# Kernel optimization log

Measured on AMD Instinct MI355X. Metric: run time of the kernel, lower is better.

Reference implementation:

```python
import jax, jax.numpy as jnp
import numpy as np

PROCESSING_SPEED = 8.0  # init kwarg: softmax temperature
EPS = 1e-8              # torch F.cosine_similarity eps
BATCH, SIZE, DIM = 1024, 65536, 512


def setup_inputs() -> dict:
    key = jax.random.key(0)
    k1, k2 = jax.random.split(key)
    x = jax.random.normal(k1, (BATCH, DIM), dtype=jnp.float32)
    memory_bank = jax.random.normal(k2, (SIZE, DIM), dtype=jnp.float32)
    return {"x": x, "memory_bank": memory_bank}


def reference(x, memory_bank):
    # Cosine similarity between every query and every memory row, computed as
    # normalized dot products (math-equivalent to F.cosine_similarity with
    # denominator clamp max(||a||*||b||, eps), avoiding the (B,S,D) broadcast).
    x_norm = jnp.linalg.norm(x, axis=1, keepdims=True)            # (B, 1)
    m_norm = jnp.linalg.norm(memory_bank, axis=1, keepdims=True)  # (S, 1)
    dots = jnp.einsum('bd,sd->bs', x, memory_bank)                # (B, S)
    sims = dots / jnp.maximum(x_norm * m_norm.T, EPS)             # (B, S)
    attention = jax.nn.softmax(sims * PROCESSING_SPEED, axis=1)   # (B, S)
    return attention @ memory_bank                                # (B, D)
```

## Files before the change

### kernel.cpp

```cpp
#include <hip/hip_runtime.h>
#include <hip/hip_bf16.h>
#include <stdint.h>

#define B_N 1024
#define S_N 65536
#define D_N 512
#define NS 32
#define SC (S_N / NS)
#define SB 128
#define NSUB (SC / SB)

typedef __attribute__((ext_vector_type(8))) short bf16x8;
typedef __attribute__((ext_vector_type(4))) float f32x4;

#define OFF_MBF   ((size_t)0)
#define OFF_MT    (OFF_MBF + (size_t)S_N * D_N * 2)
#define OFF_XBF   (OFF_MT  + (size_t)D_N * S_N * 2)
#define OFF_RX    (OFF_XBF + (size_t)B_N * D_N * 2)
#define OFF_RM    (OFF_RX  + (size_t)B_N * 4)
#define OFF_LSUM  (OFF_RM  + (size_t)S_N * 4)
#define OFF_OPART (OFF_LSUM + (size_t)B_N * 4)

__device__ __forceinline__ unsigned short f2bf(float f) {
  unsigned u = __builtin_bit_cast(unsigned, f);
  u += 0x7fffu + ((u >> 16) & 1u);
  return (unsigned short)(u >> 16);
}

__device__ __forceinline__ void stage16(const unsigned short* g, unsigned short* l) {
  __builtin_amdgcn_global_load_lds(
      (const __attribute__((address_space(1))) void*)g,
      (__attribute__((address_space(3))) void*)l, 16, 0, 0);
}

__global__ void k_prep_x(const float* __restrict__ X, unsigned short* __restrict__ Xbf,
                         float* __restrict__ rx) {
  const int row = blockIdx.x;
  const int t = threadIdx.x;
  float4 v = ((const float4*)(X + (size_t)row * D_N))[t];
  float ss = v.x*v.x + v.y*v.y + v.z*v.z + v.w*v.w;
  ushort4 o; o.x = f2bf(v.x); o.y = f2bf(v.y); o.z = f2bf(v.z); o.w = f2bf(v.w);
  ((ushort4*)(Xbf + (size_t)row * D_N))[t] = o;
  #pragma unroll
  for (int m = 1; m < 64; m <<= 1) ss += __shfl_xor(ss, m);
  __shared__ float partial[2];
  if ((t & 63) == 0) partial[t >> 6] = ss;
  __syncthreads();
  if (t == 0) rx[row] = 11.541560327111707f * rsqrtf(fmaxf(partial[0] + partial[1], 1e-24f));
}

__global__ void k_prep_m(const float* __restrict__ M, unsigned short* __restrict__ Mbf,
                         unsigned short* __restrict__ Mt, float* __restrict__ rm) {
  __shared__ float ts[64 * 65];
  const int t = threadIdx.x;
  const int s0 = blockIdx.x * 64;
  const int r = t >> 2, cq = t & 3;
  const int c = t >> 2, sq = t & 3;
  float ss = 0.f;
  for (int ct = 0; ct < 8; ++ct) {
    float f[16];
    const float4* src = (const float4*)(M + (size_t)(s0 + r) * D_N + ct * 64 + cq * 16);
    #pragma unroll
    for (int k = 0; k < 4; ++k) {
      float4 v = src[k];
      f[4*k+0] = v.x; f[4*k+1] = v.y; f[4*k+2] = v.z; f[4*k+3] = v.w;
    }
    union { unsigned short u[16]; uint4 v4[2]; } pk;
    #pragma unroll
    for (int j = 0; j < 16; ++j) {
      ss += f[j] * f[j];
      pk.u[j] = f2bf(f[j]);
      ts[r * 65 + cq * 16 + j] = f[j];
    }
    uint4* dst = (uint4*)(Mbf + (size_t)(s0 + r) * D_N + ct * 64 + cq * 16);
    dst[0] = pk.v4[0]; dst[1] = pk.v4[1];
    __syncthreads();
    union { unsigned short u[16]; uint4 v4[2]; } pt;
    #pragma unroll
    for (int j = 0; j < 16; ++j) pt.u[j] = f2bf(ts[(sq * 16 + j) * 65 + c]);
    uint4* dt = (uint4*)(Mt + (size_t)(ct * 64 + c) * S_N + s0 + sq * 16);
    dt[0] = pt.v4[0]; dt[1] = pt.v4[1];
    __syncthreads();
  }
  ss += __shfl_xor(ss, 1);
  ss += __shfl_xor(ss, 2);
  if (cq == 0) rm[s0 + r] = rsqrtf(fmaxf(ss, 1e-24f));
}

__global__ __launch_bounds__(512, 2) void k_fused(
    const unsigned short* __restrict__ Xbf, const unsigned short* __restrict__ Mbf,
    const unsigned short* __restrict__ Mt, const float* __restrict__ rx,
    const float* __restrict__ rminv, float* __restrict__ lsum,
    float* __restrict__ Opart) {
  __shared__ unsigned short smem[16384];
  __shared__ unsigned short Ps[16384];

  const int t = threadIdx.x;
  const int w = t >> 6, lane = t & 63, quad = lane >> 4, l15 = lane & 15;
  const int qr = w >> 1, qc = w & 1;
  const int x7 = l15 & 7;

  const int bid = blockIdx.x;
  const int xcd = bid & 7, slot = bid >> 3;
  const int bblk = slot & 7;
  const int chunk = xcd * 4 + (slot >> 3);
  const int b0 = bblk * 128;
  const int s0 = chunk * SC;

  unsigned short* As = smem;
  unsigned short* Bs = smem + 8192;

  f32x4 accO[4][2][4];
  #pragma unroll
  for (int dc = 0; dc < 4; ++dc)
    #pragma unroll
    for (int i = 0; i < 2; ++i)
      #pragma unroll
      for (int j = 0; j < 4; ++j) accO[dc][i][j] = (f32x4){0.f, 0.f, 0.f, 0.f};

  float ls[4] = {0.f, 0.f, 0.f, 0.f};
  float rxj[4];
  #pragma unroll
  for (int j = 0; j < 4; ++j) rxj[j] = rx[b0 + qc * 64 + j * 16 + l15];

  const int srow8 = t >> 3;
  const int sch8  = ((t & 7) ^ (srow8 & 7)) * 8;
  const unsigned short* gX = Xbf + (size_t)(b0 + srow8) * D_N + sch8;
  const int mrow = t >> 4;
  const int mch  = ((t & 15) ^ (mrow & 7)) * 8;

  for (int sub = 0; sub < NSUB; ++sub) {
    const int sS = s0 + sub * SB;

    f32x4 accP[2][4];
    #pragma unroll
    for (int i = 0; i < 2; ++i)
      #pragma unroll
      for (int j = 0; j < 4; ++j) accP[i][j] = (f32x4){0.f, 0.f, 0.f, 0.f};

    const unsigned short* gM = Mbf + (size_t)(sS + srow8) * D_N + sch8;
    for (int k0 = 0; k0 < D_N; k0 += 64) {
      stage16(gM + k0,                      As + w * 512);
      stage16(gM + (size_t)64 * D_N + k0,   As + 4096 + w * 512);
      stage16(gX + k0,                      Bs + w * 512);
      stage16(gX + (size_t)64 * D_N + k0,   Bs + 4096 + w * 512);
      __syncthreads();
      #pragma unroll
      for (int kk = 0; kk < 64; kk += 32) {
        const int cq = (kk >> 3) + quad;
        bf16x8 a[2], b[4];
        #pragma unroll
        for (int i = 0; i < 2; ++i)
          a[i] = *(const bf16x8*)&As[(qr * 32 + i * 16 + l15) * 64 + ((cq ^ x7) << 3)];
        #pragma unroll
        for (int j = 0; j < 4; ++j)
          b[j] = *(const bf16x8*)&Bs[(qc * 64 + j * 16 + l15) * 64 + ((cq ^ x7) << 3)];
        #pragma unroll
        for (int i = 0; i < 2; ++i)
          #pragma unroll
          for (int j = 0; j < 4; ++j)
            accP[i][j] = __builtin_amdgcn_mfma_f32_16x16x32_bf16(a[i], b[j], accP[i][j], 0, 0, 0);
      }
      __syncthreads();
    }

    const float4 rm0 = *(const float4*)&rminv[sS + qr * 32 + quad * 4];
    const float4 rm1 = *(const float4*)&rminv[sS + qr * 32 + 16 + quad * 4];
    #pragma unroll
    for (int i = 0; i < 2; ++i) {
      const float4 rm = i ? rm1 : rm0;
      const int sl  = qr * 32 + i * 16 + quad * 4;
      const int c16 = sl >> 3;
      const int o8  = (sl >> 2) & 1;
      #pragma unroll
      for (int j = 0; j < 4; ++j) {
        const float p0 = exp2f(accP[i][j][0] * rxj[j] * rm.x);
        const float p1 = exp2f(accP[i][j][1] * rxj[j] * rm.y);
        const float p2 = exp2f(accP[i][j][2] * rxj[j] * rm.z);
        const float p3 = exp2f(accP[i][j][3] * rxj[j] * rm.w);
        ls[j] += (p0 + p1) + (p2 + p3);
        const int brow = qc * 64 + j * 16 + l15;
        uint2 pk;
        pk.x = (unsigned)f2bf(p0) | ((unsigned)f2bf(p1) << 16);
        pk.y = (unsigned)f2bf(p2) | ((unsigned)f2bf(p3) << 16);
        *(uint2*)&Ps[brow * 128 + (((c16 ^ (brow & 7)) << 3) | (o8 << 2))] = pk;
      }
    }
    __syncthreads();

    #pragma unroll
    for (int dc = 0; dc < 4; ++dc) {
      const unsigned short* gT = Mt + (size_t)(dc * 128 + mrow) * S_N + sS + mch;
      stage16(gT,                      smem + w * 512);
      stage16(gT + (size_t)32 * S_N,   smem + 4096 + w * 512);
      stage16(gT + (size_t)64 * S_N,   smem + 8192 + w * 512);
      stage16(gT + (size_t)96 * S_N,   smem + 12288 + w * 512);
      __syncthreads();
      #pragma unroll
      for (int kk = 0; kk < 128; kk += 32) {
        const int cq = (kk >> 3) + quad;
        bf16x8 pa[2], mb[4];
        #pragma unroll
        for (int i = 0; i < 2; ++i)
          pa[i] = *(const bf16x8*)&Ps[(qr * 32 + i * 16 + l15) * 128 + ((cq ^ x7) << 3)];
        #pragma unroll
        for (int j = 0; j < 4; ++j)
          mb[j] = *(const bf16x8*)&smem[(qc * 64 + j * 16 + l15) * 128 + ((cq ^ x7) << 3)];
        #pragma unroll
        for (int i = 0; i < 2; ++i)
          #pragma unroll
          for (int j = 0; j < 4; ++j)
            accO[dc][i][j] = __builtin_amdgcn_mfma_f32_16x16x32_bf16(pa[i], mb[j], accO[dc][i][j], 0, 0, 0);
      }
      __syncthreads();
    }
  }

  float* Od = Opart + (size_t)chunk * ((size_t)B_N * D_N);
  #pragma unroll
  for (int dc = 0; dc < 4; ++dc)
    #pragma unroll
    for (int i = 0; i < 2; ++i)
      #pragma unroll
      for (int r = 0; r < 4; ++r) {
        const int bb = b0 + qr * 32 + i * 16 + quad * 4 + r;
        #pragma unroll
        for (int j = 0; j < 4; ++j) {
          const int d = dc * 128 + qc * 64 + j * 16 + l15;
          Od[(size_t)bb * D_N + d] = accO[dc][i][j][r];
        }
      }

  __syncthreads();
  float* red = (float*)smem;
  #pragma unroll
  for (int j = 0; j < 4; ++j) {
    float v = ls[j];
    v += __shfl_xor(v, 16);
    v += __shfl_xor(v, 32);
    if (lane < 16) red[w * 64 + j * 16 + lane] = v;
  }
  __syncthreads();
  if (t < 128) {
    const int qc2 = t >> 6, idx = t & 63;
    float s = red[(0 + qc2) * 64 + idx] + red[(2 + qc2) * 64 + idx] +
              red[(4 + qc2) * 64 + idx] + red[(6 + qc2) * 64 + idx];
    unsafeAtomicAdd(&lsum[b0 + t], s);
  }
}

__global__ void k_combine(const float* __restrict__ Opart, const float* __restrict__ lsum,
                          float* __restrict__ out) {
  const int idx = blockIdx.x * 256 + threadIdx.x;
  const int b = idx >> 7;
  float4 s = {0.f, 0.f, 0.f, 0.f};
  #pragma unroll
  for (int ks = 0; ks < NS; ++ks) {
    float4 v = ((const float4*)Opart)[(size_t)ks * (B_N * D_N / 4) + idx];
    s.x += v.x; s.y += v.y; s.z += v.z; s.w += v.w;
  }
  const float inv = 1.0f / lsum[b];
  s.x *= inv; s.y *= inv; s.z *= inv; s.w *= inv;
  ((float4*)out)[idx] = s;
}

extern "C" void kernel_launch(void* const* d_in, const int* in_sizes, int n_in,
                              void* d_out, int out_size, void* d_ws, size_t ws_size,
                              hipStream_t stream) {
  const float* X = (const float*)d_in[0];
  const float* M = (const float*)d_in[1];
  char* ws = (char*)d_ws;
  unsigned short* Mbf = (unsigned short*)(ws + OFF_MBF);
  unsigned short* Mt  = (unsigned short*)(ws + OFF_MT);
  unsigned short* Xbf = (unsigned short*)(ws + OFF_XBF);
  float* rxv  = (float*)(ws + OFF_RX);
  float* rmv  = (float*)(ws + OFF_RM);
  float* lsum = (float*)(ws + OFF_LSUM);
  float* Opart = (float*)(ws + OFF_OPART);

  hipMemsetAsync(lsum, 0, B_N * sizeof(float), stream);
  k_prep_x<<<dim3(B_N), 128, 0, stream>>>(X, Xbf, rxv);
  k_prep_m<<<dim3(S_N / 64), 256, 0, stream>>>(M, Mbf, Mt, rmv);
  k_fused<<<dim3(8 * NS), 512, 0, stream>>>(Xbf, Mbf, Mt, rxv, rmv, lsum, Opart);
  k_combine<<<dim3(B_N * D_N / 4 / 256), 256, 0, stream>>>(Opart, lsum, (float*)d_out);
}
```

Baseline: 468.8 us.

## Double-buffer async staging with 32x32 MFMA tiles and larger S sub-block

Rewrites the fused attention kernel's main loop so global-to-LDS staging is double-buffered with explicit vmcnt waits and raw s_barrier, prefetching the next phase (including across the QK to PV boundary and into the next sub-block) while MFMAs run. Switches from 16x16x32 to 32x32x16 bf16 MFMA tiles, doubles the S sub-block to 256, and re-partitions the PV output across waves with new swizzled layouts. Adds s_setprio around compute. The aim is to hide memory latency and cut barrier and LDS traffic per FLOP, at the cost of more LDS (about 160KB per block) and register pressure, which may reduce occupancy with launch_bounds(512,2).

```diff
diff --git a/kernel.cpp b/kernel.cpp
--- a/kernel.cpp
+++ b/kernel.cpp
@@ -7,11 +7,12 @@
 #define D_N 512
 #define NS 32
 #define SC (S_N / NS)
-#define SB 128
+#define SB 256
 #define NSUB (SC / SB)
 
 typedef __attribute__((ext_vector_type(8))) short bf16x8;
 typedef __attribute__((ext_vector_type(4))) float f32x4;
+typedef __attribute__((ext_vector_type(16))) float f32x16;
 
 #define OFF_MBF   ((size_t)0)
 #define OFF_MT    (OFF_MBF + (size_t)S_N * D_N * 2)
@@ -92,13 +93,18 @@
     const unsigned short* __restrict__ Mt, const float* __restrict__ rx,
     const float* __restrict__ rminv, float* __restrict__ lsum,
     float* __restrict__ Opart) {
-  __shared__ unsigned short smem[16384];
-  __shared__ unsigned short Ps[16384];
+  __shared__ unsigned short Stg[2][24576];
+  __shared__ unsigned short Ps[32768];
 
   const int t = threadIdx.x;
-  const int w = t >> 6, lane = t & 63, quad = lane >> 4, l15 = lane & 15;
-  const int qr = w >> 1, qc = w & 1;
-  const int x7 = l15 & 7;
+  const int w = t >> 6, lane = t & 63, l31 = lane & 31, hi = lane >> 5;
+  const int qs = w >> 1, qcb = w & 1;
+  const int hb = w >> 2, qd = w & 3;
+  const int r7 = (l31 >> 1) & 7;
+  const int p7 = l31 & 7;
+  const int t3 = l31 & 3;
+  const int sub8 = (lane & 1) * 8;
+  const int rp15 = l31 >> 1;
 
   const int bid = blockIdx.x;
   const int xcd = bid & 7, slot = bid >> 3;
@@ -107,138 +113,162 @@
   const int b0 = bblk * 128;
   const int s0 = chunk * SC;
 
-  unsigned short* As = smem;
-  unsigned short* Bs = smem + 8192;
-
-  f32x4 accO[4][2][4];
-  #pragma unroll
-  for (int dc = 0; dc < 4; ++dc)
-    #pragma unroll
-    for (int i = 0; i < 2; ++i)
-      #pragma unroll
-      for (int j = 0; j < 4; ++j) accO[dc][i][j] = (f32x4){0.f, 0.f, 0.f, 0.f};
-
-  float ls[4] = {0.f, 0.f, 0.f, 0.f};
-  float rxj[4];
-  #pragma unroll
-  for (int j = 0; j < 4; ++j) rxj[j] = rx[b0 + qc * 64 + j * 16 + l15];
-
-  const int srow8 = t >> 3;
-  const int sch8  = ((t & 7) ^ (srow8 & 7)) * 8;
-  const unsigned short* gX = Xbf + (size_t)(b0 + srow8) * D_N + sch8;
-  const int mrow = t >> 4;
-  const int mch  = ((t & 15) ^ (mrow & 7)) * 8;
+  const int mrow_t = ((t >> 4) << 1) | (t & 1);
+  const int mc8    = ((((t >> 1) & 7) ^ ((t >> 4) & 7)) << 3);
+  const int trow_t = t >> 2;
+  const int tc8    = (((t & 3) ^ ((t >> 2) & 3)) << 3);
+
+  #define ISS_QK(sS_, k0_, bi_) do {                                           \
+    _Pragma("unroll")                                                          \
+    for (int is = 0; is < 4; ++is)                                             \
+      stage16(Mbf + (size_t)((sS_) + is * 64 + mrow_t) * D_N + (k0_) + mc8,    \
+              &Stg[bi_][is * 4096 + w * 512]);                                 \
+    _Pragma("unroll")                                                          \
+    for (int is = 0; is < 2; ++is)                                             \
+      stage16(Xbf + (size_t)(b0 + is * 64 + mrow_t) * D_N + (k0_) + mc8,       \
+              &Stg[bi_][16384 + is * 4096 + w * 512]);                         \
+  } while (0)
+  #define ISS_T(sS_, ph_, bi_) do {                                            \
+    _Pragma("unroll")                                                          \
+    for (int is = 0; is < 4; ++is)                                             \
+      stage16(Mt + (size_t)(is * 128 + trow_t) * S_N + (sS_) + (ph_) * 32 + tc8, \
+              &Stg[bi_][is * 4096 + w * 512]);                                 \
+  } while (0)
+
+  f32x16 accO[2][4];
+  #pragma unroll
+  for (int i = 0; i < 2; ++i)
+    #pragma unroll
+    for (int j = 0; j < 4; ++j)
+      #pragma unroll
+      for (int r = 0; r < 16; ++r) accO[i][j][r] = 0.f;
+
+  float ls[2] = {0.f, 0.f};
+  float rxj[2];
+  #pragma unroll
+  for (int j = 0; j < 2; ++j) rxj[j] = rx[b0 + qcb * 64 + j * 32 + l31];
+
+  ISS_QK(s0, 0, 0);
 
   for (int sub = 0; sub < NSUB; ++sub) {
     const int sS = s0 + sub * SB;
 
-    f32x4 accP[2][4];
+    f32x16 accP[2][2];
     #pragma unroll
     for (int i = 0; i < 2; ++i)
       #pragma unroll
-      for (int j = 0; j < 4; ++j) accP[i][j] = (f32x4){0.f, 0.f, 0.f, 0.f};
-
-    const unsigned short* gM = Mbf + (size_t)(sS + srow8) * D_N + sch8;
-    for (int k0 = 0; k0 < D_N; k0 += 64) {
-      stage16(gM + k0,                      As + w * 512);
-      stage16(gM + (size_t)64 * D_N + k0,   As + 4096 + w * 512);
-      stage16(gX + k0,                      Bs + w * 512);
-      stage16(gX + (size_t)64 * D_N + k0,   Bs + 4096 + w * 512);
-      __syncthreads();
-      #pragma unroll
-      for (int kk = 0; kk < 64; kk += 32) {
-        const int cq = (kk >> 3) + quad;
-        bf16x8 a[2], b[4];
+      for (int j = 0; j < 2; ++j)
+        #pragma unroll
+        for (int r = 0; r < 16; ++r) accP[i][j][r] = 0.f;
+
+    #pragma unroll
+    for (int ph = 0; ph < 8; ++ph) {
+      const int bi = ph & 1;
+      if (ph < 7) { ISS_QK(sS, (ph + 1) * 64, bi ^ 1); }
+      else        { ISS_T(sS, 0, bi ^ 1); }
+      if (ph < 7) asm volatile("s_waitcnt vmcnt(6)" ::: "memory");
+      else        asm volatile("s_waitcnt vmcnt(4)" ::: "memory");
+      __builtin_amdgcn_s_barrier();
+      const unsigned short* Ms = &Stg[bi][0];
+      const unsigned short* Xs = &Stg[bi][16384];
+      __builtin_amdgcn_s_setprio(1);
+      #pragma unroll
+      for (int ks = 0; ks < 4; ++ks) {
+        const int c = ks * 2 + hi;
+        bf16x8 aB[2], xB[2];
         #pragma unroll
         for (int i = 0; i < 2; ++i)
-          a[i] = *(const bf16x8*)&As[(qr * 32 + i * 16 + l15) * 64 + ((cq ^ x7) << 3)];
+          aB[i] = *(const bf16x8*)&Ms[(qs * 32 + i * 16 + rp15) * 128 + ((c ^ r7) << 4) + sub8];
+        #pragma unroll
+        for (int j = 0; j < 2; ++j)
+          xB[j] = *(const bf16x8*)&Xs[(qcb * 32 + j * 16 + rp15) * 128 + ((c ^ r7) << 4) + sub8];
+        #pragma unroll
+        for (int i = 0; i < 2; ++i)
+          #pragma unroll
+          for (int j = 0; j < 2; ++j)
+            accP[i][j] = __builtin_amdgcn_mfma_f32_32x32x16_bf16(aB[i], xB[j], accP[i][j], 0, 0, 0);
+      }
+      __builtin_amdgcn_s_setprio(0);
+      __builtin_amdgcn_s_barrier();
+    }
+
+    #pragma unroll
+    for (int i = 0; i < 2; ++i)
+      #pragma unroll
+      for (int g = 0; g < 4; ++g) {
+        const float4 rm = *(const float4*)&rminv[sS + qs * 64 + i * 32 + g * 8 + hi * 4];
+        const int c16 = qs * 8 + i * 4 + g;
+        #pragma unroll
+        for (int j = 0; j < 2; ++j) {
+          const float p0 = exp2f(accP[i][j][g * 4 + 0] * rxj[j] * rm.x);
+          const float p1 = exp2f(accP[i][j][g * 4 + 1] * rxj[j] * rm.y);
+          const float p2 = exp2f(accP[i][j][g * 4 + 2] * rxj[j] * rm.z);
+          const float p3 = exp2f(accP[i][j][g * 4 + 3] * rxj[j] * rm.w);
+          ls[j] += (p0 + p1) + (p2 + p3);
+          const int brow = qcb * 64 + j * 32 + l31;
+          uint2 pk;
+          pk.x = (unsigned)f2bf(p0) | ((unsigned)f2bf(p1) << 16);
+          pk.y = (unsigned)f2bf(p2) | ((unsigned)f2bf(p3) << 16);
+          *(uint2*)&Ps[brow * 256 + ((c16 ^ p7) << 3) + hi * 4] = pk;
+        }
+      }
+    asm volatile("s_waitcnt lgkmcnt(0)" ::: "memory");
+
+    #pragma unroll
+    for (int ph = 0; ph < 8; ++ph) {
+      const int bi = ph & 1;
+      if (ph < 7)                { ISS_T(sS, ph + 1, bi ^ 1); }
+      else if (sub < NSUB - 1)   { ISS_QK(sS + SB, 0, bi ^ 1); }
+      if (ph < 7)                     asm volatile("s_waitcnt vmcnt(4)" ::: "memory");
+      else if (sub < NSUB - 1)        asm volatile("s_waitcnt vmcnt(6)" ::: "memory");
+      else                            asm volatile("s_waitcnt vmcnt(0)" ::: "memory");
+      __builtin_amdgcn_s_barrier();
+      const unsigned short* Ts = &Stg[bi][0];
+      __builtin_amdgcn_s_setprio(1);
+      #pragma unroll
+      for (int ks = 0; ks < 2; ++ks) {
+        const int cP = ph * 4 + ks * 2 + hi;
+        const int cT = ks * 2 + hi;
+        bf16x8 pa[2], mB[4];
+        #pragma unroll
+        for (int i = 0; i < 2; ++i)
+          pa[i] = *(const bf16x8*)&Ps[(hb * 64 + i * 32 + l31) * 256 + ((cP ^ p7) << 3)];
         #pragma unroll
         for (int j = 0; j < 4; ++j)
-          b[j] = *(const bf16x8*)&Bs[(qc * 64 + j * 16 + l15) * 64 + ((cq ^ x7) << 3)];
+          mB[j] = *(const bf16x8*)&Ts[(qd * 128 + j * 32 + l31) * 32 + ((cT ^ t3) << 3)];
         #pragma unroll
         for (int i = 0; i < 2; ++i)
           #pragma unroll
           for (int j = 0; j < 4; ++j)
-            accP[i][j] = __builtin_amdgcn_mfma_f32_16x16x32_bf16(a[i], b[j], accP[i][j], 0, 0, 0);
+            accO[i][j] = __builtin_amdgcn_mfma_f32_32x32x16_bf16(pa[i], mB[j], accO[i][j], 0, 0, 0);
       }
-      __syncthreads();
+      __builtin_amdgcn_s_setprio(0);
+      __builtin_amdgcn_s_barrier();
     }
-
-    const float4 rm0 = *(const float4*)&rminv[sS + qr * 32 + quad * 4];
-    const float4 rm1 = *(const float4*)&rminv[sS + qr * 32 + 16 + quad * 4];
-    #pragma unroll
-    for (int i = 0; i < 2; ++i) {
-      const float4 rm = i ? rm1 : rm0;
-      const int sl  = qr * 32 + i * 16 + quad * 4;
-      const int c16 = sl >> 3;
-      const int o8  = (sl >> 2) & 1;
-      #pragma unroll
-      for (int j = 0; j < 4; ++j) {
-        const float p0 = exp2f(accP[i][j][0] * rxj[j] * rm.x);
-        const float p1 = exp2f(accP[i][j][1] * rxj[j] * rm.y);
-        const float p2 = exp2f(accP[i][j][2] * rxj[j] * rm.z);
-        const float p3 = exp2f(accP[i][j][3] * rxj[j] * rm.w);
-        ls[j] += (p0 + p1) + (p2 + p3);
-        const int brow = qc * 64 + j * 16 + l15;
-        uint2 pk;
-        pk.x = (unsigned)f2bf(p0) | ((unsigned)f2bf(p1) << 16);
-        pk.y = (unsigned)f2bf(p2) | ((unsigned)f2bf(p3) << 16);
-        *(uint2*)&Ps[brow * 128 + (((c16 ^ (brow & 7)) << 3) | (o8 << 2))] = pk;
-      }
-    }
-    __syncthreads();
-
-    #pragma unroll
-    for (int dc = 0; dc < 4; ++dc) {
-      const unsigned short* gT = Mt + (size_t)(dc * 128 + mrow) * S_N + sS + mch;
-      stage16(gT,                      smem + w * 512);
-      stage16(gT + (size_t)32 * S_N,   smem + 4096 + w * 512);
-      stage16(gT + (size_t)64 * S_N,   smem + 8192 + w * 512);
-      stage16(gT + (size_t)96 * S_N,   smem + 12288 + w * 512);
-      __syncthreads();
-      #pragma unroll
-      for (int kk = 0; kk < 128; kk += 32) {
-        const int cq = (kk >> 3) + quad;
-        bf16x8 pa[2], mb[4];
-        #pragma unroll
-        for (int i = 0; i < 2; ++i)
-          pa[i] = *(const bf16x8*)&Ps[(qr * 32 + i * 16 + l15) * 128 + ((cq ^ x7) << 3)];
-        #pragma unroll
-        for (int j = 0; j < 4; ++j)
-          mb[j] = *(const bf16x8*)&smem[(qc * 64 + j * 16 + l15) * 128 + ((cq ^ x7) << 3)];
-        #pragma unroll
-        for (int i = 0; i < 2; ++i)
-          #pragma unroll
-          for (int j = 0; j < 4; ++j)
-            accO[dc][i][j] = __builtin_amdgcn_mfma_f32_16x16x32_bf16(pa[i], mb[j], accO[dc][i][j], 0, 0, 0);
-      }
-      __syncthreads();
-    }
   }
 
   float* Od = Opart + (size_t)chunk * ((size_t)B_N * D_N);
   #pragma unroll
-  for (int dc = 0; dc < 4; ++dc)
-    #pragma unroll
-    for (int i = 0; i < 2; ++i)
+  for (int i = 0; i < 2; ++i)
+    #pragma unroll
+    for (int g = 0; g < 4; ++g)
       #pragma unroll
       for (int r = 0; r < 4; ++r) {
-        const int bb = b0 + qr * 32 + i * 16 + quad * 4 + r;
+        const int bb = b0 + hb * 64 + i * 32 + g * 8 + hi * 4 + r;
         #pragma unroll
         for (int j = 0; j < 4; ++j) {
-          const int d = dc * 128 + qc * 64 + j * 16 + l15;
-          Od[(size_t)bb * D_N + d] = accO[dc][i][j][r];
+          const int d = qd * 128 + j * 32 + l31;
+          Od[(size_t)bb * D_N + d] = accO[i][j][g * 4 + r];
         }
       }
 
   __syncthreads();
-  float* red = (float*)smem;
-  #pragma unroll
-  for (int j = 0; j < 4; ++j) {
+  float* red = (float*)&Stg[0][0];
+  #pragma unroll
+  for (int j = 0; j < 2; ++j) {
     float v = ls[j];
-    v += __shfl_xor(v, 16);
     v += __shfl_xor(v, 32);
-    if (lane < 16) red[w * 64 + j * 16 + lane] = v;
+    if (lane < 32) red[w * 64 + j * 32 + l31] = v;
   }
   __syncthreads();
   if (t < 128) {
@@ -247,6 +277,8 @@
               red[(4 + qc2) * 64 + idx] + red[(6 + qc2) * 64 + idx];
     unsafeAtomicAdd(&lsum[b0 + t], s);
   }
+  #undef ISS_QK
+  #undef ISS_T
 }
 
 __global__ void k_combine(const float* __restrict__ Opart, const float* __restrict__ lsum,
```

Result: slower. 489.3 us (+4.4%).
